# Kernel tuning notes

Hardware: AMD Instinct MI355X
Metric: run time of the kernel (lower is better)

## Reference

```python
import jax, jax.numpy as jnp
import numpy as np

B, Q, C, H, W = 2, 10, 64, 256, 256   # input is (B*Q, C, H, W); N ico nodes = Q*H*W
K = 9                                  # KNN kernel size
L_H, L_W = 180, 360                    # ERP grid (180/delta x 360/delta), delta=1
L = L_H * L_W
N = Q * H * W


def setup_inputs() -> dict:
    key = jax.random.key(0)
    k1, k2, k3, k4, k5, k6 = jax.random.split(key, 6)
    x = jax.random.normal(k1, (B * Q, C, H, W), dtype=jnp.float32)
    idx = jax.random.randint(k2, (L, K), 0, N, dtype=jnp.int64)  # zero-based seqnumkmin
    att_w = jax.random.normal(k3, (K, 2, K), dtype=jnp.float32) * 0.1  # Conv2d(2,K,(1,K)) weight
    att_b = jax.random.normal(k4, (K,), dtype=jnp.float32) * 0.1
    tc_w = jax.random.normal(k5, (C, K), dtype=jnp.float32) * 0.1     # depthwise Conv2d(C,C,(1,K),groups=C)
    tc_b = jax.random.normal(k6, (C,), dtype=jnp.float32) * 0.1
    return {"x": x, "idx": idx, "att_w": att_w, "att_b": att_b, "tc_w": tc_w, "tc_b": tc_b}


def reference(x, idx, att_w, att_b, tc_w, tc_b):
    # (b q) c h w -> b c (q h w)
    b = x.shape[0] // Q
    xf = x.reshape(b, Q, C, H, W).transpose(0, 2, 1, 3, 4).reshape(b, C, N)
    # KNN gather: (b, C, L, K)
    xe = xf[:, :, idx]
    # spatial attention: mean/max over channels -> (b, 2, L, K)
    stats = jnp.stack([xe.mean(axis=1), xe.max(axis=1)], axis=1)
    # conv (1,K) over neighbor axis: out (b, K, L)
    att = jax.nn.sigmoid(jnp.einsum('bilk,cik->bcl', stats, att_w) + att_b[None, :, None])
    att = att.transpose(0, 2, 1)[:, None, :, :]  # b 1 L K
    xe = att * xe + xe
    # depthwise grouped conv over neighbor axis -> (b, C, L)
    out = jnp.einsum('bclk,ck->bcl', xe, tc_w) + tc_b[None, :, None]
    return out.reshape(b, C, L_H, L_W)
```

## Files before the change

### kernel.cpp

```cpp
#include <hip/hip_runtime.h>
#include <hip/hip_bf16.h>
#include <math.h>

#define QQ   10
#define CC   64
#define HWSZ 65536
#define NPOS 655360
#define LL   64800
#define KK   9

__global__ __launch_bounds__(256) void k_transpose_stats(
    const float* __restrict__ x, __hip_bfloat16* __restrict__ xt,
    float* __restrict__ s, float* __restrict__ m) {
  __shared__ float tile[64][65];
  __shared__ float sred[4][64];
  __shared__ float mred[4][64];
  const int t    = threadIdx.x;
  const int lane = t & 63;
  const int wid  = t >> 6;
  const int hw_base = blockIdx.x * 64;
  const int bq = blockIdx.y;
  const float* xp = x + (size_t)bq * CC * HWSZ + hw_base;

#pragma unroll
  for (int i = 0; i < 4; ++i) {
    int linear = t + i * 256;
    int row  = linear >> 4;
    int col4 = (linear & 15) << 2;
    const float4 v = *(const float4*)(xp + (size_t)row * HWSZ + col4);
    tile[row][col4 + 0] = v.x;
    tile[row][col4 + 1] = v.y;
    tile[row][col4 + 2] = v.z;
    tile[row][col4 + 3] = v.w;
  }
  __syncthreads();

  const int b = bq / QQ, q = bq % QQ;
  const size_t n_base = (size_t)q * HWSZ + hw_base;
  __hip_bfloat16* xtb = xt + (size_t)b * NPOS * CC;
  float* sb  = s  + (size_t)b * NPOS;
  float* mb  = m  + (size_t)b * NPOS;

#pragma unroll 4
  for (int i = 0; i < 16; ++i) {
    const int nl = wid * 16 + i;
    const size_t n = n_base + nl;
    xtb[n * CC + lane] = __float2bfloat16(tile[lane][nl]);
  }

  {
    const int pos = lane;
    const int c0  = wid * 16;
    float psum = tile[c0][pos];
    float pmax = psum;
#pragma unroll
    for (int c = 1; c < 16; ++c) {
      const float v = tile[c0 + c][pos];
      psum += v;
      pmax = fmaxf(pmax, v);
    }
    sred[wid][pos] = psum;
    mred[wid][pos] = pmax;
  }
  __syncthreads();
  if (wid == 0) {
    const int pos = lane;
    const float sum = sred[0][pos] + sred[1][pos] + sred[2][pos] + sred[3][pos];
    const float mx  = fmaxf(fmaxf(mred[0][pos], mred[1][pos]),
                            fmaxf(mred[2][pos], mred[3][pos]));
    sb[n_base + pos] = sum;
    mb[n_base + pos] = mx;
  }
}

__global__ __launch_bounds__(256) void k_gather_out(
    const __hip_bfloat16* __restrict__ xt, const float* __restrict__ s,
    const float* __restrict__ m, const int* __restrict__ idx,
    const float* __restrict__ att_w, const float* __restrict__ att_b,
    const float* __restrict__ tc_w, const float* __restrict__ tc_b,
    float* __restrict__ out) {
  const int blk    = blockIdx.x;
  const int b      = blk / (LL / 16);
  const int l_base = (blk % (LL / 16)) * 16;
  const int t = threadIdx.x, lane = t & 63, wid = t >> 6;
  __shared__ float res[64][17];

  float tcw[KK];
#pragma unroll
  for (int k = 0; k < KK; ++k) tcw[k] = tc_w[lane * KK + k];
  const float tcb = tc_b[lane];

  const int c9 = lane < KK ? lane : 0;
  float aw0[KK], aw1[KK];
#pragma unroll
  for (int k = 0; k < KK; ++k) {
    aw0[k] = att_w[c9 * 2 * KK + k];
    aw1[k] = att_w[c9 * 2 * KK + KK + k];
  }
  const float ab = att_b[c9];

  const __hip_bfloat16* xtb = xt + (size_t)b * NPOS * CC;
  const float* sb  = s  + (size_t)b * NPOS;
  const float* mb  = m  + (size_t)b * NPOS;

#pragma unroll
  for (int j = 0; j < 4; ++j) {
    const int l = l_base + wid * 4 + j;
    const int kl = lane < KK ? lane : KK - 1;
    const int nk = idx[l * KK + kl];
    const float sv = sb[nk];
    const float mv = mb[nk];

    float logit = ab;
#pragma unroll
    for (int k = 0; k < KK; ++k) {
      const float mean = __shfl(sv, k) * (1.0f / 64.0f);
      const float mx   = __shfl(mv, k);
      logit = fmaf(mean, aw0[k], logit);
      logit = fmaf(mx,   aw1[k], logit);
    }
    const float w = 1.0f + 1.0f / (1.0f + __expf(-logit));

    float acc = 0.0f;
#pragma unroll
    for (int k = 0; k < KK; ++k) {
      const int   n  = __shfl(nk, k);
      const float wk = __shfl(w, k);
      const float v  = __bfloat162float(xtb[(size_t)n * CC + lane]);
      acc = fmaf(wk * tcw[k], v, acc);
    }
    res[lane][wid * 4 + j] = acc + tcb;
  }
  __syncthreads();

  const int c  = t >> 2;
  const int j4 = t & 3;
  float4 o;
  o.x = res[c][j4 * 4 + 0];
  o.y = res[c][j4 * 4 + 1];
  o.z = res[c][j4 * 4 + 2];
  o.w = res[c][j4 * 4 + 3];
  *(float4*)(out + ((size_t)b * CC + c) * LL + l_base + j4 * 4) = o;
}

extern "C" void kernel_launch(void* const* d_in, const int* in_sizes, int n_in,
                              void* d_out, int out_size, void* d_ws, size_t ws_size,
                              hipStream_t stream) {
  const float* x     = (const float*)d_in[0];
  const int*   idx   = (const int*)d_in[1];
  const float* att_w = (const float*)d_in[2];
  const float* att_b = (const float*)d_in[3];
  const float* tc_w  = (const float*)d_in[4];
  const float* tc_b  = (const float*)d_in[5];
  float* out = (float*)d_out;

  __hip_bfloat16* xt = (__hip_bfloat16*)d_ws;
  float* s  = (float*)(xt + (size_t)2 * NPOS * CC);
  float* mm = s + (size_t)2 * NPOS;

  dim3 g1(HWSZ / 64, 2 * QQ);
  k_transpose_stats<<<g1, 256, 0, stream>>>(x, xt, s, mm);

  dim3 g2(2 * (LL / 16));
  k_gather_out<<<g2, 256, 0, stream>>>(xt, s, mm, idx, att_w, att_b,
                                       tc_w, tc_b, out);
}
```

Measured before the change: 534.8 us.

## Split attention into separate kernel, pack stats, vectorize bf16 stores and gathers

Interleaves sum and max stats into one float2 array so each neighbor's stats come from a single load. Moves the attention-logit computation into its own kernel that writes per-(b,l,k) weights to workspace. The gather kernel now reads two bf16 channels per 32-bit load, so each wavefront handles two output positions, with 32 positions per block. The transpose kernel writes packed 8-byte bf16 chunks instead of 2-byte scalars. The extra kernel launch and the round trip of attention weights through memory trade against fewer shuffles and wider memory accesses.

```diff
diff --git a/kernel.cpp b/kernel.cpp
--- a/kernel.cpp
+++ b/kernel.cpp
@@ -11,7 +11,7 @@
 
 __global__ __launch_bounds__(256) void k_transpose_stats(
     const float* __restrict__ x, __hip_bfloat16* __restrict__ xt,
-    float* __restrict__ s, float* __restrict__ m) {
+    float2* __restrict__ stats) {
   __shared__ float tile[64][65];
   __shared__ float sred[4][64];
   __shared__ float mred[4][64];
@@ -38,24 +38,31 @@
   const int b = bq / QQ, q = bq % QQ;
   const size_t n_base = (size_t)q * HWSZ + hw_base;
   __hip_bfloat16* xtb = xt + (size_t)b * NPOS * CC;
-  float* sb  = s  + (size_t)b * NPOS;
-  float* mb  = m  + (size_t)b * NPOS;
-
-#pragma unroll 4
-  for (int i = 0; i < 16; ++i) {
-    const int nl = wid * 16 + i;
-    const size_t n = n_base + nl;
-    xtb[n * CC + lane] = __float2bfloat16(tile[lane][nl]);
+
+  const int c0  = (lane & 15) << 2;
+  const int sub = lane >> 4;
+#pragma unroll
+  for (int j = 0; j < 4; ++j) {
+    const int p = wid * 16 + j * 4 + sub;
+    const float v0 = tile[c0 + 0][p];
+    const float v1 = tile[c0 + 1][p];
+    const float v2 = tile[c0 + 2][p];
+    const float v3 = tile[c0 + 3][p];
+    union { __hip_bfloat162 h; unsigned u; } lo, hi;
+    lo.h = __float22bfloat162_rn(make_float2(v0, v1));
+    hi.h = __float22bfloat162_rn(make_float2(v2, v3));
+    uint2 pk; pk.x = lo.u; pk.y = hi.u;
+    *(uint2*)(xtb + (n_base + p) * CC + c0) = pk;
   }
 
   {
     const int pos = lane;
-    const int c0  = wid * 16;
-    float psum = tile[c0][pos];
+    const int cc0 = wid * 16;
+    float psum = tile[cc0][pos];
     float pmax = psum;
 #pragma unroll
     for (int c = 1; c < 16; ++c) {
-      const float v = tile[c0 + c][pos];
+      const float v = tile[cc0 + c][pos];
       psum += v;
       pmax = fmaxf(pmax, v);
     }
@@ -65,82 +72,112 @@
   __syncthreads();
   if (wid == 0) {
     const int pos = lane;
-    const float sum = sred[0][pos] + sred[1][pos] + sred[2][pos] + sred[3][pos];
-    const float mx  = fmaxf(fmaxf(mred[0][pos], mred[1][pos]),
-                            fmaxf(mred[2][pos], mred[3][pos]));
-    sb[n_base + pos] = sum;
-    mb[n_base + pos] = mx;
+    float2 sm;
+    sm.x = sred[0][pos] + sred[1][pos] + sred[2][pos] + sred[3][pos];
+    sm.y = fmaxf(fmaxf(mred[0][pos], mred[1][pos]),
+                 fmaxf(mred[2][pos], mred[3][pos]));
+    stats[(size_t)b * NPOS + n_base + pos] = sm;
+  }
+}
+
+__global__ __launch_bounds__(256) void k_att(
+    const float2* __restrict__ stats, const int* __restrict__ idx,
+    const float* __restrict__ att_w, const float* __restrict__ att_b,
+    float* __restrict__ watt) {
+  __shared__ float aw[2 * KK * KK + KK];
+  const int t = threadIdx.x;
+  if (t < 2 * KK * KK) aw[t] = att_w[t];
+  else if (t < 2 * KK * KK + KK) aw[t] = att_b[t - 2 * KK * KK];
+  __syncthreads();
+
+  const int tg = blockIdx.x * 256 + t;
+  if (tg >= 2 * LL) return;
+  const int b = tg / LL;
+  const int l = tg - b * LL;
+  const float2* st = stats + (size_t)b * NPOS;
+
+  float mean[KK], mx[KK];
+#pragma unroll
+  for (int k = 0; k < KK; ++k) {
+    const int n = idx[l * KK + k];
+    const float2 sm = st[n];
+    mean[k] = sm.x * (1.0f / 64.0f);
+    mx[k]   = sm.y;
+  }
+
+  float* wp = watt + (size_t)tg * KK;
+#pragma unroll
+  for (int h = 0; h < KK; ++h) {
+    float logit = aw[2 * KK * KK + h];
+#pragma unroll
+    for (int k = 0; k < KK; ++k) {
+      logit = fmaf(mean[k], aw[h * 2 * KK + k], logit);
+      logit = fmaf(mx[k],   aw[h * 2 * KK + KK + k], logit);
+    }
+    wp[h] = 1.0f + 1.0f / (1.0f + __expf(-logit));
   }
 }
 
 __global__ __launch_bounds__(256) void k_gather_out(
-    const __hip_bfloat16* __restrict__ xt, const float* __restrict__ s,
-    const float* __restrict__ m, const int* __restrict__ idx,
-    const float* __restrict__ att_w, const float* __restrict__ att_b,
-    const float* __restrict__ tc_w, const float* __restrict__ tc_b,
-    float* __restrict__ out) {
+    const __hip_bfloat16* __restrict__ xt, const int* __restrict__ idx,
+    const float* __restrict__ watt, const float* __restrict__ tc_w,
+    const float* __restrict__ tc_b, float* __restrict__ out) {
   const int blk    = blockIdx.x;
-  const int b      = blk / (LL / 16);
-  const int l_base = (blk % (LL / 16)) * 16;
+  const int b      = blk / (LL / 32);
+  const int l_base = (blk % (LL / 32)) * 32;
   const int t = threadIdx.x, lane = t & 63, wid = t >> 6;
-  __shared__ float res[64][17];
-
-  float tcw[KK];
-#pragma unroll
-  for (int k = 0; k < KK; ++k) tcw[k] = tc_w[lane * KK + k];
-  const float tcb = tc_b[lane];
-
-  const int c9 = lane < KK ? lane : 0;
-  float aw0[KK], aw1[KK];
+  const int half = lane >> 5, lh = lane & 31;
+  __shared__ float res[64][33];
+
+  float tw0[KK], tw1[KK];
 #pragma unroll
   for (int k = 0; k < KK; ++k) {
-    aw0[k] = att_w[c9 * 2 * KK + k];
-    aw1[k] = att_w[c9 * 2 * KK + KK + k];
-  }
-  const float ab = att_b[c9];
-
-  const __hip_bfloat16* xtb = xt + (size_t)b * NPOS * CC;
-  const float* sb  = s  + (size_t)b * NPOS;
-  const float* mb  = m  + (size_t)b * NPOS;
+    tw0[k] = tc_w[(2 * lh) * KK + k];
+    tw1[k] = tc_w[(2 * lh + 1) * KK + k];
+  }
+  const float tb0 = tc_b[2 * lh];
+  const float tb1 = tc_b[2 * lh + 1];
+
+  const unsigned* xtb = (const unsigned*)(xt + (size_t)b * NPOS * CC);
+  const float* wb = watt + (size_t)b * LL * KK;
+  const int kl = lh < KK ? lh : KK - 1;
 
 #pragma unroll
   for (int j = 0; j < 4; ++j) {
-    const int l = l_base + wid * 4 + j;
-    const int kl = lane < KK ? lane : KK - 1;
-    const int nk = idx[l * KK + kl];
-    const float sv = sb[nk];
-    const float mv = mb[nk];
-
-    float logit = ab;
+    const int myl = l_base + wid * 8 + j * 2 + half;
+    const int   nk = idx[myl * KK + kl];
+    const float wv = wb[myl * KK + kl];
+
+    float a0 = 0.0f, a1 = 0.0f;
 #pragma unroll
     for (int k = 0; k < KK; ++k) {
-      const float mean = __shfl(sv, k) * (1.0f / 64.0f);
-      const float mx   = __shfl(mv, k);
-      logit = fmaf(mean, aw0[k], logit);
-      logit = fmaf(mx,   aw1[k], logit);
+      const int   src = half * 32 + k;
+      const int   n   = __shfl(nk, src);
+      const float wk  = __shfl(wv, src);
+      const unsigned u = xtb[(size_t)n * 32 + lh];
+      const float f0 = __uint_as_float(u << 16);
+      const float f1 = __uint_as_float(u & 0xffff0000u);
+      a0 = fmaf(wk * tw0[k], f0, a0);
+      a1 = fmaf(wk * tw1[k], f1, a1);
     }
-    const float w = 1.0f + 1.0f / (1.0f + __expf(-logit));
-
-    float acc = 0.0f;
-#pragma unroll
-    for (int k = 0; k < KK; ++k) {
-      const int   n  = __shfl(nk, k);
-      const float wk = __shfl(w, k);
-      const float v  = __bfloat162float(xtb[(size_t)n * CC + lane]);
-      acc = fmaf(wk * tcw[k], v, acc);
-    }
-    res[lane][wid * 4 + j] = acc + tcb;
+    const int li = wid * 8 + j * 2 + half;
+    res[2 * lh][li]     = a0 + tb0;
+    res[2 * lh + 1][li] = a1 + tb1;
   }
   __syncthreads();
 
   const int c  = t >> 2;
-  const int j4 = t & 3;
-  float4 o;
-  o.x = res[c][j4 * 4 + 0];
-  o.y = res[c][j4 * 4 + 1];
-  o.z = res[c][j4 * 4 + 2];
-  o.w = res[c][j4 * 4 + 3];
-  *(float4*)(out + ((size_t)b * CC + c) * LL + l_base + j4 * 4) = o;
+  const int q4 = t & 3;
+#pragma unroll
+  for (int rep = 0; rep < 2; ++rep) {
+    const int lo = rep * 16 + q4 * 4;
+    float4 o;
+    o.x = res[c][lo + 0];
+    o.y = res[c][lo + 1];
+    o.z = res[c][lo + 2];
+    o.w = res[c][lo + 3];
+    *(float4*)(out + ((size_t)b * CC + c) * LL + l_base + lo) = o;
+  }
 }
 
 extern "C" void kernel_launch(void* const* d_in, const int* in_sizes, int n_in,
@@ -155,13 +192,15 @@
   float* out = (float*)d_out;
 
   __hip_bfloat16* xt = (__hip_bfloat16*)d_ws;
-  float* s  = (float*)(xt + (size_t)2 * NPOS * CC);
-  float* mm = s + (size_t)2 * NPOS;
+  float2* stats = (float2*)(xt + (size_t)2 * NPOS * CC);
+  float* watt = (float*)(stats + (size_t)2 * NPOS);
 
   dim3 g1(HWSZ / 64, 2 * QQ);
-  k_transpose_stats<<<g1, 256, 0, stream>>>(x, xt, s, mm);
-
-  dim3 g2(2 * (LL / 16));
-  k_gather_out<<<g2, 256, 0, stream>>>(xt, s, mm, idx, att_w, att_b,
-                                       tc_w, tc_b, out);
-}
+  k_transpose_stats<<<g1, 256, 0, stream>>>(x, xt, stats);
+
+  dim3 g2((2 * LL + 255) / 256);
+  k_att<<<g2, 256, 0, stream>>>(stats, idx, att_w, att_b, watt);
+
+  dim3 g3(2 * (LL / 32));
+  k_gather_out<<<g3, 256, 0, stream>>>(xt, idx, watt, tc_w, tc_b, out);
+}
```

Measured after the change: 548.5 us. 2.6% more time.
